# Kernel optimization log

Hardware: AMD Instinct MI355X
Metric: run time of the kernel (lower is better)

## Reference

```python
import jax, jax.numpy as jnp
import numpy as np

IO = 1024
D_SLOT = 128
SCALES = [1, 2, 4]
N = 4          # lcm of scales (streams / period)
K = 3          # number of scales (active slots per step)
S = 7          # sum of scales (total slots)
D = D_SLOT * S # 896, per-stream dim
H = K * N      # 12 heads
RANK = 256
HID = 3584
B, T = 4, 1024
EPS = 1e-5


def _tables():
    # active_slots[phase, scale_idx] -> slot id
    act = np.zeros((N, K), dtype=np.int32)
    for p in range(N):
        off = 0
        for i, s in enumerate(SCALES):
            act[p, i] = off + p % s
            off += s
    # head_assignments[stream, slot] -> head id (SHARED mode)
    ha = np.zeros((N, S), dtype=np.int32)
    off = 0
    for i, s in enumerate(SCALES):
        alpha = N // s
        for j in range(s):
            ha[:, off + j] = i * N + (np.arange(N) + alpha * j) % N
        off += s
    return act, ha

ACTIVE_SLOTS, HEAD_ASSIGN = _tables()


def layernorm(x, g, b):
    m = jnp.mean(x, axis=-1, keepdims=True)
    v = jnp.mean(jnp.square(x - m), axis=-1, keepdims=True)
    return (x - m) * jax.lax.rsqrt(v + EPS) * g + b


def setup_inputs() -> dict:
    key = jax.random.key(0)
    ks = jax.random.split(key, 16)
    f32 = jnp.float32
    return {
        'x': jax.random.normal(ks[0], (B, T, IO), f32),
        't': 3,
        'enc_base_w': jax.random.normal(ks[1], (D, IO), f32) * 0.02,
        'enc_A_w': jax.random.normal(ks[2], (RANK, IO), f32) * 0.02,
        'enc_B': jax.random.normal(ks[3], (RANK, N, D), f32) * 0.02,
        'enc_beta': jnp.asarray(0.01, f32),
        'ln_mixer_g': jnp.ones((D,), f32),
        'ln_mixer_b': jnp.zeros((D,), f32),
        'mix_w1': jax.random.normal(ks[4], (HID, D), f32) * 0.02,
        'mix_b1': jnp.zeros((HID,), f32),
        'mix_w2': jax.random.normal(ks[5], (D, HID), f32) * 0.02,
        'mix_b2': jnp.zeros((D,), f32),
        'ln_attn_g': jnp.ones((D,), f32),
        'ln_attn_b': jnp.zeros((D,), f32),
        'Wq': jax.random.normal(ks[6], (H, D, D_SLOT), f32) * 0.02,
        'Wk': jax.random.normal(ks[7], (H, D, D_SLOT), f32) * 0.02,
        'Wv': jax.random.normal(ks[8], (H, D, D_SLOT), f32) * 0.02,
        'dec_ln_g': jnp.ones((N * D,), f32),
        'dec_ln_b': jnp.zeros((N * D,), f32),
        'dec_down_w': jax.random.normal(ks[9], (RANK, N * D), f32) * 0.02,
        'dec_up_w': jax.random.normal(ks[10], (IO, RANK), f32) * 0.02,
    }


def reference(x, t, enc_base_w, enc_A_w, enc_B, enc_beta,
              ln_mixer_g, ln_mixer_b, mix_w1, mix_b1, mix_w2, mix_b2,
              ln_attn_g, ln_attn_b, Wq, Wk, Wv,
              dec_ln_g, dec_ln_b, dec_down_w, dec_up_w):
    b, tt, _ = x.shape
    # --- StreamLoRAEncoder: x [B,T,IO] -> z [B,T,N,D] ---
    base = x @ enc_base_w.T                       # [B,T,D]
    h = x @ enc_A_w.T                             # [B,T,RANK]
    delta = jnp.einsum('btr,rnd->btnd', h, enc_B) # [B,T,N,D]
    z = base[:, :, None, :] + enc_beta * delta

    # --- step(z, t, is_causal=True) ---
    phase = int(t) % N
    active = ACTIVE_SLOTS[phase]                               # [K]
    head_ids = HEAD_ASSIGN[np.arange(N)[:, None], active[None, :]]  # [N,K]

    # mixer (pre-LN MLP residual)
    zm = layernorm(z, ln_mixer_g, ln_mixer_b)
    m = jax.nn.gelu(zm @ mix_w1.T + mix_b1, approximate=False) @ mix_w2.T + mix_b2
    z_head = z + m                                             # [B,T,N,D]

    # per-head multi-scale attention; head input scope = STREAM (full D)
    hin = layernorm(z_head, ln_attn_g, ln_attn_b)              # [B,T,N,D]
    Wq_s, Wk_s, Wv_s = Wq[head_ids], Wk[head_ids], Wv[head_ids]  # [N,K,D,d]
    q = jnp.einsum('btnc,nkcd->btnkd', hin, Wq_s)
    k = jnp.einsum('btnc,nkcd->btnkd', hin, Wk_s)
    v = jnp.einsum('btnc,nkcd->btnkd', hin, Wv_s)
    scale = 1.0 / jnp.sqrt(jnp.asarray(D_SLOT, q.dtype))
    scores = jnp.einsum('bqnkd,bpnkd->bnkqp', q, k) * scale    # [B,N,K,T,T]
    causal = jnp.tril(jnp.ones((tt, tt), dtype=bool))
    scores = jnp.where(causal, scores, jnp.finfo(scores.dtype).min)
    attn = jax.nn.softmax(scores, axis=-1)
    out = jnp.einsum('bnkqp,bpnkd->bqnkd', attn, v)            # [B,T,N,K,d]

    # write attention outputs back into the active slots (residual)
    z_slots = z_head.reshape(b, tt, N, S, D_SLOT)
    z_new = z_slots.at[:, :, :, jnp.asarray(active), :].add(out)
    z_new = z_new.reshape(b, tt, N, D)

    # --- StreamLoRADecoder: z [B,T,N,D] -> y [B,T,IO] ---
    cat = z_new.reshape(b, tt, N * D)
    c = layernorm(cat, dec_ln_g, dec_ln_b)
    y = (c @ dec_down_w.T) @ dec_up_w.T
    return y
```

## Files before the change

### kernel.cpp

```cpp
#include <hip/hip_runtime.h>
#include <hip/hip_bf16.h>
#include <math.h>

typedef __hip_bfloat16 bf16;
typedef __attribute__((ext_vector_type(8))) short v8s;
typedef __attribute__((ext_vector_type(4))) float v4f;

#define EPI_F32    0
#define EPI_BF16   1
#define EPI_GELU   2
#define EPI_RESID  3
#define EPI_RESID0 4
#define EPI_WZ     5
#define EPI_ATOM   6
#define EPI_VT     7

__device__ __forceinline__ float bf_lo(unsigned int w) { return __uint_as_float(w << 16); }
__device__ __forceinline__ float bf_hi(unsigned int w) { return __uint_as_float(w & 0xffff0000u); }
__device__ __forceinline__ unsigned short f2b_bits(float f) {
  unsigned int u = __float_as_uint(f);
  unsigned int r = (u + 0x7fffu + ((u >> 16) & 1u)) >> 16;
  return (unsigned short)r;
}
__device__ __forceinline__ void unpack8(uint4 u, float* f) {
  unsigned int w0 = u.x, w1 = u.y, w2 = u.z, w3 = u.w;
  f[0] = bf_lo(w0); f[1] = bf_hi(w0);
  f[2] = bf_lo(w1); f[3] = bf_hi(w1);
  f[4] = bf_lo(w2); f[5] = bf_hi(w2);
  f[6] = bf_lo(w3); f[7] = bf_hi(w3);
}
__device__ __forceinline__ void load8(const float* p, float* f) {
  float4 a = ((const float4*)p)[0];
  float4 b = ((const float4*)p)[1];
  f[0] = a.x; f[1] = a.y; f[2] = a.z; f[3] = a.w;
  f[4] = b.x; f[5] = b.y; f[6] = b.z; f[7] = b.w;
}
__device__ __forceinline__ void gl_lds16(const void* g, void* l) {
  __builtin_amdgcn_global_load_lds(
      (__attribute__((address_space(1))) void*)g,
      (__attribute__((address_space(3))) void*)l, 16, 0, 0);
}

__global__ __launch_bounds__(256) void cvt_kernel(const float* __restrict__ src,
                                                  bf16* __restrict__ dst, int n)
{
  int i = (blockIdx.x * 256 + threadIdx.x) * 8;
  if (i >= n) return;
  float f[8]; load8(src + i, f);
  unsigned short us[8];
#pragma unroll
  for (int j = 0; j < 8; j++) us[j] = f2b_bits(f[j]);
  *(uint4*)((unsigned short*)dst + i) = *(uint4*)us;
}

__global__ __launch_bounds__(256) void cvt_t_kernel(const float* __restrict__ src,
                                                    bf16* __restrict__ dst, int R, int C)
{
  __shared__ float tile[32][33];
  const int c0 = blockIdx.x * 32, r0 = blockIdx.y * 32;
  const size_t bo = (size_t)blockIdx.z * R * C;
  const int tx = threadIdx.x & 31, ty = threadIdx.x >> 5;
#pragma unroll
  for (int i = 0; i < 4; i++) {
    int r = ty * 4 + i;
    tile[r][tx] = src[bo + (size_t)(r0 + r) * C + c0 + tx];
  }
  __syncthreads();
#pragma unroll
  for (int i = 0; i < 4; i++) {
    int r = ty * 4 + i;
    *((unsigned short*)dst + bo + (size_t)(c0 + r) * R + r0 + tx) = f2b_bits(tile[tx][r]);
  }
}

__device__ __forceinline__ void stage_async(const bf16* __restrict__ src, int ld, int r0, int k0,
                                            bf16* lds, int wave, int lane)
{
#pragma unroll
  for (int t = 0; t < 2; t++) {
    int seg = wave * 2 + t;
    const bf16* g = src + (size_t)(r0 + seg * 16 + (lane >> 2)) * ld + k0 + (lane & 3) * 8;
    gl_lds16(g, lds + seg * 512);
  }
}
__device__ __forceinline__ void stage_sync(const float* __restrict__ src, int ld, int r0, int k0,
                                           bf16* lds, int tid)
{
#pragma unroll
  for (int t = 0; t < 2; t++) {
    int s = t * 256 + tid;
    int m = s >> 2, c = s & 3;
    float f[8]; load8(src + (size_t)(r0 + m) * ld + k0 + c * 8, f);
    unsigned short us[8];
#pragma unroll
    for (int j = 0; j < 8; j++) us[j] = f2b_bits(f[j]);
    *(uint4*)&lds[m * 32 + c * 8] = *(uint4*)us;
  }
}
__device__ __forceinline__ void stage_tile(const bf16* __restrict__ src, int ld, int r0, int k0,
                                           bf16* lds, int tid, int wave, int lane)
{ stage_async(src, ld, r0, k0, lds, wave, lane); }
__device__ __forceinline__ void stage_tile(const float* __restrict__ src, int ld, int r0, int k0,
                                           bf16* lds, int tid, int wave, int lane)
{ stage_sync(src, ld, r0, k0, lds, tid); }

template<typename TA, typename TB, int EPI>
__device__ void mfma_core(const TA* __restrict__ A, int lda,
                          const TB* __restrict__ B, int ldb,
                          void* __restrict__ C, int ldc,
                          const float* __restrict__ bias,
                          const float* __restrict__ beta_p,
                          int m0, int n0, int K)
{
  __shared__ bf16 As[128 * 32];
  __shared__ bf16 Bs[128 * 32];
  const int tid = threadIdx.x;
  const int lane = tid & 63, wave = tid >> 6;
  const int mw = (wave & 1) * 64, nw = (wave >> 1) * 64;
  const int row = lane & 15, kc = lane >> 4;

  v4f acc[4][4];
  const v4f vzero = {0.f, 0.f, 0.f, 0.f};
#pragma unroll
  for (int i = 0; i < 4; i++)
#pragma unroll
    for (int j = 0; j < 4; j++) acc[i][j] = vzero;

  for (int k0 = 0; k0 < K; k0 += 32) {
    stage_tile(A, lda, m0, k0, As, tid, wave, lane);
    stage_tile(B, ldb, n0, k0, Bs, tid, wave, lane);
    __syncthreads();
    v8s af[4], bfr[4];
#pragma unroll
    for (int i = 0; i < 4; i++)
      af[i] = *(const v8s*)&As[(mw + i * 16 + row) * 32 + kc * 8];
#pragma unroll
    for (int j = 0; j < 4; j++)
      bfr[j] = *(const v8s*)&Bs[(nw + j * 16 + row) * 32 + kc * 8];
#pragma unroll
    for (int i = 0; i < 4; i++)
#pragma unroll
      for (int j = 0; j < 4; j++)
        acc[i][j] = __builtin_amdgcn_mfma_f32_16x16x32_bf16(af[i], bfr[j], acc[i][j], 0, 0, 0);
    __syncthreads();
  }

  const int cl = lane & 15, rq = lane >> 4;
  if (EPI == EPI_VT) {
#pragma unroll
    for (int mi = 0; mi < 4; mi++) {
#pragma unroll
      for (int nj = 0; nj < 4; nj++) {
        const int col = n0 + nw + nj * 16 + cl;
        const int rb = m0 + mw + mi * 16 + rq * 4;
        unsigned short us[4];
#pragma unroll
        for (int i = 0; i < 4; i++) us[i] = f2b_bits(acc[mi][nj][i]);
        *(ushort2*)((unsigned short*)C + (size_t)col * 4096 + rb) = *(ushort2*)us;
        *(ushort2*)((unsigned short*)C + (size_t)col * 4096 + rb + 2) = *(ushort2*)(us + 2);
      }
    }
    return;
  }
  const float beta = (EPI == EPI_WZ) ? beta_p[0] : 0.f;
#pragma unroll
  for (int mi = 0; mi < 4; mi++) {
#pragma unroll
    for (int nj = 0; nj < 4; nj++) {
      const int col = n0 + nw + nj * 16 + cl;
#pragma unroll
      for (int i = 0; i < 4; i++) {
        const int r = m0 + mw + mi * 16 + rq * 4 + i;
        float v = acc[mi][nj][i];
        if (EPI == EPI_F32) {
          ((float*)C)[(size_t)r * ldc + col] = v;
        } else if (EPI == EPI_BF16) {
          ((unsigned short*)C)[(size_t)r * ldc + col] = f2b_bits(v);
        } else if (EPI == EPI_GELU) {
          v += bias[col];
          v = 0.5f * v * (1.f + erff(v * 0.70710678118654752f));
          ((unsigned short*)C)[(size_t)r * ldc + col] = f2b_bits(v);
        } else if (EPI == EPI_RESID) {
          float* Z = (float*)C;
          size_t idx = (size_t)r * ldc + col;
          Z[idx] = Z[idx] + v + bias[col];
        } else if (EPI == EPI_RESID0) {
          float* Z = (float*)C;
          size_t idx = (size_t)r * ldc + col;
          Z[idx] = Z[idx] + v;
        } else if (EPI == EPI_WZ) {
          float o = beta * v + bias[(size_t)(r % 896) * 1024 + col];
          ((unsigned short*)C)[(size_t)r * ldc + col] = f2b_bits(o);
        } else if (EPI == EPI_ATOM) {
          float add = v + (bias ? bias[col] : 0.f);
          atomicAdd(&((float*)C)[(size_t)r * ldc + col], add);
        }
      }
    }
  }
}

template<typename TA, typename TB, int EPI>
__global__ __launch_bounds__(256) void mfma_gemm(const TA* __restrict__ A, int lda,
                                                 const TB* __restrict__ B, int ldb,
                                                 void* __restrict__ C, int ldc,
                                                 const float* __restrict__ bias,
                                                 const float* __restrict__ beta_p, int K)
{
  mfma_core<TA, TB, EPI>(A, lda, B, ldb, C, ldc, bias, beta_p,
                         blockIdx.y * 128, blockIdx.x * 128, K);
}

template<typename TA, typename TB, int EPI>
__global__ __launch_bounds__(256) void mfma_gemm_sw(const TA* __restrict__ A, int lda,
                                                    const TB* __restrict__ B, int ldb,
                                                    void* __restrict__ C, int ldc,
                                                    const float* __restrict__ bias,
                                                    const float* __restrict__ beta_p, int K)
{
  const int lin = blockIdx.x;
  const int m0 = ((((lin & 7) << 4) | ((lin >> 3) & 15))) * 128;
  const int n0 = (lin >> 7) * 128;
  mfma_core<TA, TB, EPI>(A, lda, B, ldb, C, ldc, bias, beta_p, m0, n0, K);
}

template<typename TA, typename TB>
__global__ __launch_bounds__(256) void mfma_gemm_sk_sw(const TA* __restrict__ A, int lda,
                                                       const TB* __restrict__ B, int ldb,
                                                       float* __restrict__ C, int ldc,
                                                       const float* __restrict__ bias, int Kc)
{
  const int chunk = blockIdx.x & 1;
  const int l2 = blockIdx.x >> 1;
  const int m0 = ((((l2 & 7) << 4) | ((l2 >> 3) & 15))) * 128;
  const int n0 = (l2 >> 7) * 128;
  const int kofs = chunk * Kc;
  mfma_core<TA, TB, EPI_ATOM>(A + kofs, lda, B + kofs, ldb, C, ldc,
                              (chunk == 0) ? bias : nullptr, nullptr, m0, n0, Kc);
}

template<typename TA, typename TB>
__global__ __launch_bounds__(256) void mfma_gemm_sk(const TA* __restrict__ A, int lda,
                                                    const TB* __restrict__ B, int ldb,
                                                    float* __restrict__ C, int ldc,
                                                    const float* __restrict__ bias, int Kc)
{
  const int kofs = blockIdx.z * Kc;
  mfma_core<TA, TB, EPI_ATOM>(A + kofs, lda, B + kofs, ldb, C, ldc,
                              (blockIdx.z == 0) ? bias : nullptr, nullptr,
                              blockIdx.y * 128, blockIdx.x * 128, Kc);
}

__global__ __launch_bounds__(256) void qkv_mfma(const bf16* __restrict__ hin,
                                                const bf16* __restrict__ Wt,
                                                bf16* __restrict__ qkv,
                                                const int* __restrict__ tptr)
{
  const int zb = blockIdx.z;
  const int type = zb / 12, rem = zb % 12, n = rem / 3, kh = rem % 3;
  const int phase = ((tptr[0] % 4) + 4) % 4;
  const int hid = (kh == 0) ? n
                : (kh == 1) ? 4 + (n + 2 * (phase & 1)) % 4
                            : 8 + (n + phase) % 4;
  const bf16* B = Wt + ((size_t)type * 12 + hid) * 128 * 896;
  bf16* out = qkv + ((size_t)type * 12 + n * 3 + kh) * 4096 * 128;
  mfma_core<bf16, bf16, EPI_BF16>(hin + n * 896, 3584, B, 896, out, 128,
                                  nullptr, nullptr, blockIdx.y * 128, 0, 896);
}

__global__ __launch_bounds__(256) void qkv_v_mfma(const bf16* __restrict__ hin,
                                                  const bf16* __restrict__ Wt,
                                                  bf16* __restrict__ vt,
                                                  const int* __restrict__ tptr)
{
  const int rem = blockIdx.z, n = rem / 3, kh = rem % 3;
  const int phase = ((tptr[0] % 4) + 4) % 4;
  const int hid = (kh == 0) ? n
                : (kh == 1) ? 4 + (n + 2 * (phase & 1)) % 4
                            : 8 + (n + phase) % 4;
  const bf16* B = Wt + ((size_t)2 * 12 + hid) * 128 * 896;
  bf16* out = vt + (size_t)(n * 3 + kh) * 128 * 4096;
  mfma_core<bf16, bf16, EPI_VT>(hin + n * 896, 3584, B, 896, out, 0,
                                nullptr, nullptr, blockIdx.y * 128, 0, 896);
}

__global__ __launch_bounds__(256) void ln_kernel(const float* __restrict__ in,
                                                 const float* __restrict__ g,
                                                 const float* __restrict__ bsh,
                                                 bf16* __restrict__ out, int D)
{
  __shared__ float row[3584];
  __shared__ float red[256];
  const int tid = threadIdx.x;
  const size_t base = (size_t)blockIdx.x * D;
  float s = 0.f;
  for (int i = tid; i < D; i += 256) { float v = in[base + i]; row[i] = v; s += v; }
  red[tid] = s; __syncthreads();
  for (int o = 128; o > 0; o >>= 1) { if (tid < o) red[tid] += red[tid + o]; __syncthreads(); }
  const float mean = red[0] / (float)D;
  __syncthreads();
  s = 0.f;
  for (int i = tid; i < D; i += 256) { float d = row[i] - mean; s += d * d; }
  red[tid] = s; __syncthreads();
  for (int o = 128; o > 0; o >>= 1) { if (tid < o) red[tid] += red[tid + o]; __syncthreads(); }
  const float inv = rsqrtf(red[0] / (float)D + 1e-5f);
  for (int i = tid; i < D; i += 256) {
    float v = (row[i] - mean) * inv * g[i] + bsh[i];
    *((unsigned short*)out + base + i) = f2b_bits(v);
  }
}

__global__ __launch_bounds__(256) void attn_mfma(const bf16* __restrict__ qkv,
                                                 const bf16* __restrict__ vt,
                                                 float* __restrict__ z,
                                                 const int* __restrict__ tptr)
{
  __shared__ bf16 Ks[64 * 136];
  __shared__ bf16 Vs[128 * 72];
  __shared__ bf16 Ps[4][16 * 72];
  const int tid = threadIdx.x;
  const int lane = tid & 63, wave = tid >> 6;
  const int cl = lane & 15, rq = lane >> 4;
  const int qb = 15 - blockIdx.x;
  const int bnk = blockIdx.y;
  const int b = bnk / 12, rem = bnk % 12, n = rem / 3, kh = rem % 3;
  const int phase = ((tptr[0] % 4) + 4) % 4;
  const int slot = (kh == 0) ? 0 : (kh == 1) ? 1 + (phase & 1) : 3 + phase;
  const int head = n * 3 + kh;
  const size_t HS = (size_t)12 * 4096 * 128;
  const bf16* qp = qkv + ((size_t)head * 4096 + b * 1024) * 128;
  const bf16* kp = qkv + HS + ((size_t)head * 4096 + b * 1024) * 128;
  const bf16* vtp = vt + (size_t)head * 128 * 4096;

  v8s aq[4];
  {
    const bf16* qrow = qp + (size_t)(qb * 64 + wave * 16 + cl) * 128 + rq * 8;
#pragma unroll
    for (int c = 0; c < 4; c++) aq[c] = *(const v8s*)(qrow + c * 32);
  }
  v4f oacc[8];
  const v4f vzero = {0.f, 0.f, 0.f, 0.f};
#pragma unroll
  for (int c = 0; c < 8; c++) oacc[c] = vzero;
  float m_i[4] = {-1e30f, -1e30f, -1e30f, -1e30f};
  float l_i[4] = {0.f, 0.f, 0.f, 0.f};

  for (int kt = 0; kt <= qb; kt++) {
    __syncthreads();
#pragma unroll
    for (int t = 0; t < 4; t++) {
      int s = t * 256 + tid;
      int r = s >> 4, c0 = (s & 15) * 8;
      *(uint4*)&Ks[r * 136 + c0] = *(const uint4*)(kp + (size_t)(kt * 64 + r) * 128 + c0);
    }
#pragma unroll
    for (int t = 0; t < 4; t++) {
      int s = t * 256 + tid;
      int d = s >> 3, c0 = (s & 7) * 8;
      *(uint4*)&Vs[d * 72 + c0] =
          *(const uint4*)(vtp + (size_t)d * 4096 + b * 1024 + kt * 64 + c0);
    }
    __syncthreads();

    v4f s_acc[4];
#pragma unroll
    for (int blk = 0; blk < 4; blk++) {
      s_acc[blk] = vzero;
#pragma unroll
      for (int c = 0; c < 4; c++) {
        v8s bk = *(const v8s*)&Ks[(blk * 16 + cl) * 136 + c * 32 + rq * 8];
        s_acc[blk] = __builtin_amdgcn_mfma_f32_16x16x32_bf16(aq[c], bk, s_acc[blk], 0, 0, 0);
      }
    }
#pragma unroll
    for (int blk = 0; blk < 4; blk++)
#pragma unroll
      for (int i = 0; i < 4; i++) {
        float sv = s_acc[blk][i] * 0.088388347648318447f;
        if (kt == qb && (blk * 16 + cl) > (wave * 16 + rq * 4 + i)) sv = -1e30f;
        s_acc[blk][i] = sv;
      }
    float al[4];
#pragma unroll
    for (int i = 0; i < 4; i++) {
      float mx = fmaxf(fmaxf(s_acc[0][i], s_acc[1][i]), fmaxf(s_acc[2][i], s_acc[3][i]));
      mx = fmaxf(mx, __shfl_xor(mx, 1, 64));
      mx = fmaxf(mx, __shfl_xor(mx, 2, 64));
      mx = fmaxf(mx, __shfl_xor(mx, 4, 64));
      mx = fmaxf(mx, __shfl_xor(mx, 8, 64));
      const float mn = fmaxf(m_i[i], mx);
      al[i] = __expf(m_i[i] - mn);
      m_i[i] = mn;
      float ps = 0.f;
#pragma unroll
      for (int blk = 0; blk < 4; blk++) {
        float p = __expf(s_acc[blk][i] - mn);
        s_acc[blk][i] = p;
        ps += p;
      }
      ps += __shfl_xor(ps, 1, 64);
      ps += __shfl_xor(ps, 2, 64);
      ps += __shfl_xor(ps, 4, 64);
      ps += __shfl_xor(ps, 8, 64);
      l_i[i] = l_i[i] * al[i] + ps;
    }
#pragma unroll
    for (int c = 0; c < 8; c++)
#pragma unroll
      for (int i = 0; i < 4; i++) oacc[c][i] *= al[i];
    bf16* ps = Ps[wave];
#pragma unroll
    for (int blk = 0; blk < 4; blk++)
#pragma unroll
      for (int i = 0; i < 4; i++)
        *((unsigned short*)ps + (rq * 4 + i) * 72 + blk * 16 + cl) = f2b_bits(s_acc[blk][i]);
    v8s pa[2];
#pragma unroll
    for (int c = 0; c < 2; c++)
      pa[c] = *(const v8s*)&ps[cl * 72 + c * 32 + rq * 8];
#pragma unroll
    for (int c = 0; c < 8; c++)
#pragma unroll
      for (int ch = 0; ch < 2; ch++) {
        v8s bv = *(const v8s*)&Vs[(c * 16 + cl) * 72 + ch * 32 + rq * 8];
        oacc[c] = __builtin_amdgcn_mfma_f32_16x16x32_bf16(pa[ch], bv, oacc[c], 0, 0, 0);
      }
  }
#pragma unroll
  for (int c = 0; c < 8; c++) {
    const int d = c * 16 + cl;
#pragma unroll
    for (int i = 0; i < 4; i++) {
      const int t = qb * 64 + wave * 16 + rq * 4 + i;
      float* dst = z + ((size_t)(b * 1024 + t)) * 3584 + n * 896 + slot * 128 + d;
      *dst += oacc[c][i] / l_i[i];
    }
  }
}

extern "C" void kernel_launch(void* const* d_in, const int* in_sizes, int n_in,
                              void* d_out, int out_size, void* d_ws, size_t ws_size,
                              hipStream_t stream)
{
  const float* x        = (const float*)d_in[0];
  const int*   tptr     = (const int*)d_in[1];
  const float* enc_base = (const float*)d_in[2];
  const float* enc_A    = (const float*)d_in[3];
  const float* enc_B    = (const float*)d_in[4];
  const float* beta_p   = (const float*)d_in[5];
  const float* lnm_g    = (const float*)d_in[6];
  const float* lnm_b    = (const float*)d_in[7];
  const float* w1       = (const float*)d_in[8];
  const float* b1       = (const float*)d_in[9];
  const float* w2       = (const float*)d_in[10];
  const float* b2       = (const float*)d_in[11];
  const float* lna_g    = (const float*)d_in[12];
  const float* lna_b    = (const float*)d_in[13];
  const float* Wq       = (const float*)d_in[14];
  const float* Wk       = (const float*)d_in[15];
  const float* Wv       = (const float*)d_in[16];
  const float* dln_g    = (const float*)d_in[17];
  const float* dln_b    = (const float*)d_in[18];
  const float* down_w   = (const float*)d_in[19];
  const float* up_w     = (const float*)d_in[20];

  const bool big = (ws_size >= (size_t)228458496);
  char* ws = (char*)d_ws;
  float* z = (float*)ws;
  char* ra = ws + (size_t)58720256;
  bf16 *act, *qkv, *bufb, *w1b, *w2b, *encBt, *Wt;
  if (big) {
    act   = (bf16*)ra;
    qkv   = (bf16*)ra;
    bufb  = (bf16*)(ws + (size_t)176160768);
    w1b   = (bf16*)(ws + (size_t)205520896);
    w2b   = (bf16*)(ws + (size_t)211943424);
    encBt = (bf16*)(ws + (size_t)218365952);
    Wt    = (bf16*)(ws + (size_t)220200960);
  } else {
    act   = (bf16*)ra;
    qkv   = (bf16*)ra;
    bufb  = (bf16*)(ws + (size_t)96468992);
    w1b   = (bf16*)(ws + (size_t)125829120);
    w2b   = (bf16*)(ws + (size_t)132251648);
    encBt = (bf16*)(ws + (size_t)138674176);
    Wt    = (bf16*)(ws + (size_t)140509184);
  }
  bf16* vtb = qkv + (size_t)24 * 4096 * 128;
  bf16* xb    = (bf16*)ra;
  bf16* encAt = (bf16*)(ra + (size_t)8912896);
  bf16* Wz    = (bf16*)(ra + (size_t)9437184);
  bf16* dwT   = (bf16*)ra;
  bf16* Wdec  = (bf16*)(ra + (size_t)2097152);

  dim3 blk(256);
  hipMemsetAsync(d_out, 0, (size_t)4096 * 1024 * 4, stream);

  cvt_kernel<<<1568, blk, 0, stream>>>(w1, w1b, 3211264);
  cvt_kernel<<<1568, blk, 0, stream>>>(w2, w2b, 3211264);
  cvt_kernel<<<2048, blk, 0, stream>>>(x, xb, 4194304);
  cvt_t_kernel<<<dim3(112, 8, 1), blk, 0, stream>>>(enc_B, encBt, 256, 3584);
  cvt_t_kernel<<<dim3(32, 8, 1), blk, 0, stream>>>(enc_A, encAt, 256, 1024);
  cvt_t_kernel<<<dim3(4, 28, 12), blk, 0, stream>>>(Wq, Wt,                      896, 128);
  cvt_t_kernel<<<dim3(4, 28, 12), blk, 0, stream>>>(Wk, Wt + (size_t)12*128*896, 896, 128);
  cvt_t_kernel<<<dim3(4, 28, 12), blk, 0, stream>>>(Wv, Wt + (size_t)24*128*896, 896, 128);
  mfma_gemm<bf16, bf16, EPI_WZ><<<dim3(8, 28), blk, 0, stream>>>(
      encBt, 256, encAt, 256, Wz, 1024, enc_base, beta_p, 256);

  mfma_gemm<bf16, bf16, EPI_F32><<<dim3(28, 32), blk, 0, stream>>>(
      xb, 1024, Wz, 1024, z, 3584, nullptr, nullptr, 1024);

  ln_kernel<<<dim3(16384), blk, 0, stream>>>(z, lnm_g, lnm_b, bufb, 896);

  if (big) {
    mfma_gemm_sw<bf16, bf16, EPI_GELU><<<dim3(3584), blk, 0, stream>>>(bufb, 896, w1b, 896, act, 3584, b1, nullptr, 896);
    mfma_gemm_sk_sw<bf16, bf16><<<dim3(1792), blk, 0, stream>>>(act, 3584, w2b, 3584, z, 896, b2, 1792);
  } else {
    for (int c = 0; c < 4; c++) {
      mfma_gemm_sw<bf16, bf16, EPI_GELU><<<dim3(896), blk, 0, stream>>>(
          bufb, 896, w1b + (size_t)c * 896 * 896, 896, act, 896, b1 + c * 896, nullptr, 896);
      if (c == 0)
        mfma_gemm_sw<bf16, bf16, EPI_RESID><<<dim3(896), blk, 0, stream>>>(
            act, 896, w2b + (size_t)c * 896, 3584, z, 896, b2, nullptr, 896);
      else
        mfma_gemm_sw<bf16, bf16, EPI_RESID0><<<dim3(896), blk, 0, stream>>>(
            act, 896, w2b + (size_t)c * 896, 3584, z, 896, nullptr, nullptr, 896);
    }
  }

  ln_kernel<<<dim3(16384), blk, 0, stream>>>(z, lna_g, lna_b, bufb, 896);
  qkv_mfma<<<dim3(1, 32, 24), blk, 0, stream>>>(bufb, Wt, qkv, tptr);
  qkv_v_mfma<<<dim3(1, 32, 12), blk, 0, stream>>>(bufb, Wt, vtb, tptr);
  attn_mfma<<<dim3(16, 48), blk, 0, stream>>>(qkv, vtb, z, tptr);

  cvt_t_kernel<<<dim3(112, 8, 1), blk, 0, stream>>>(down_w, dwT, 256, 3584);
  mfma_gemm<float, bf16, EPI_BF16><<<dim3(28, 8), blk, 0, stream>>>(
      up_w, 256, dwT, 256, Wdec, 3584, nullptr, nullptr, 256);

  ln_kernel<<<dim3(4096), blk, 0, stream>>>(z, dln_g, dln_b, bufb, 3584);
  mfma_gemm_sk<bf16, bf16><<<dim3(8, 32, 4), blk, 0, stream>>>(
      bufb, 3584, Wdec, 3584, (float*)d_out, 1024, nullptr, 896);
}
```

Before: 983.4 us.

## Stage 64-wide K tiles per barrier and drop split-K for mixer down-projection

The shared GEMM core now loads two 32-wide K sub-tiles into double-size LDS buffers before each barrier and runs the MFMAs over both. This halves the number of barrier round-trips per K step. The mixer's second GEMM drops the split-K atomic kernel in favour of a single-pass residual-epilogue GEMM over the full K of 3584, which removes the atomic float adds but halves the block count. The change doubles LDS use per block, which may reduce occupancy, and it assumes K is a multiple of 64 for every GEMM.

```diff
diff --git a/kernel.cpp b/kernel.cpp
--- a/kernel.cpp
+++ b/kernel.cpp
@@ -112,8 +112,8 @@
                           const float* __restrict__ beta_p,
                           int m0, int n0, int K)
 {
-  __shared__ bf16 As[128 * 32];
-  __shared__ bf16 Bs[128 * 32];
+  __shared__ bf16 As[2][128 * 32];
+  __shared__ bf16 Bs[2][128 * 32];
   const int tid = threadIdx.x;
   const int lane = tid & 63, wave = tid >> 6;
   const int mw = (wave & 1) * 64, nw = (wave >> 1) * 64;
@@ -126,22 +126,27 @@
 #pragma unroll
     for (int j = 0; j < 4; j++) acc[i][j] = vzero;
 
-  for (int k0 = 0; k0 < K; k0 += 32) {
-    stage_tile(A, lda, m0, k0, As, tid, wave, lane);
-    stage_tile(B, ldb, n0, k0, Bs, tid, wave, lane);
+  for (int k0 = 0; k0 < K; k0 += 64) {
+    stage_tile(A, lda, m0, k0,      As[0], tid, wave, lane);
+    stage_tile(A, lda, m0, k0 + 32, As[1], tid, wave, lane);
+    stage_tile(B, ldb, n0, k0,      Bs[0], tid, wave, lane);
+    stage_tile(B, ldb, n0, k0 + 32, Bs[1], tid, wave, lane);
     __syncthreads();
-    v8s af[4], bfr[4];
-#pragma unroll
-    for (int i = 0; i < 4; i++)
-      af[i] = *(const v8s*)&As[(mw + i * 16 + row) * 32 + kc * 8];
-#pragma unroll
-    for (int j = 0; j < 4; j++)
-      bfr[j] = *(const v8s*)&Bs[(nw + j * 16 + row) * 32 + kc * 8];
-#pragma unroll
-    for (int i = 0; i < 4; i++)
+#pragma unroll
+    for (int h = 0; h < 2; h++) {
+      v8s af[4], bfr[4];
+#pragma unroll
+      for (int i = 0; i < 4; i++)
+        af[i] = *(const v8s*)&As[h][(mw + i * 16 + row) * 32 + kc * 8];
 #pragma unroll
       for (int j = 0; j < 4; j++)
-        acc[i][j] = __builtin_amdgcn_mfma_f32_16x16x32_bf16(af[i], bfr[j], acc[i][j], 0, 0, 0);
+        bfr[j] = *(const v8s*)&Bs[h][(nw + j * 16 + row) * 32 + kc * 8];
+#pragma unroll
+      for (int i = 0; i < 4; i++)
+#pragma unroll
+        for (int j = 0; j < 4; j++)
+          acc[i][j] = __builtin_amdgcn_mfma_f32_16x16x32_bf16(af[i], bfr[j], acc[i][j], 0, 0, 0);
+    }
     __syncthreads();
   }
 
@@ -225,21 +230,6 @@
 }
 
 template<typename TA, typename TB>
-__global__ __launch_bounds__(256) void mfma_gemm_sk_sw(const TA* __restrict__ A, int lda,
-                                                       const TB* __restrict__ B, int ldb,
-                                                       float* __restrict__ C, int ldc,
-                                                       const float* __restrict__ bias, int Kc)
-{
-  const int chunk = blockIdx.x & 1;
-  const int l2 = blockIdx.x >> 1;
-  const int m0 = ((((l2 & 7) << 4) | ((l2 >> 3) & 15))) * 128;
-  const int n0 = (l2 >> 7) * 128;
-  const int kofs = chunk * Kc;
-  mfma_core<TA, TB, EPI_ATOM>(A + kofs, lda, B + kofs, ldb, C, ldc,
-                              (chunk == 0) ? bias : nullptr, nullptr, m0, n0, Kc);
-}
-
-template<typename TA, typename TB>
 __global__ __launch_bounds__(256) void mfma_gemm_sk(const TA* __restrict__ A, int lda,
                                                     const TB* __restrict__ B, int ldb,
                                                     float* __restrict__ C, int ldc,
@@ -514,7 +504,7 @@
 
   if (big) {
     mfma_gemm_sw<bf16, bf16, EPI_GELU><<<dim3(3584), blk, 0, stream>>>(bufb, 896, w1b, 896, act, 3584, b1, nullptr, 896);
-    mfma_gemm_sk_sw<bf16, bf16><<<dim3(1792), blk, 0, stream>>>(act, 3584, w2b, 3584, z, 896, b2, 1792);
+    mfma_gemm_sw<bf16, bf16, EPI_RESID><<<dim3(896), blk, 0, stream>>>(act, 3584, w2b, 3584, z, 896, b2, nullptr, 3584);
   } else {
     for (int c = 0; c < 4; c++) {
       mfma_gemm_sw<bf16, bf16, EPI_GELU><<<dim3(896), blk, 0, stream>>>(
```

After: 896.4 us. 1.1x faster.
